# Optimization experiments

Measured on AMD Instinct MI355X. Metric: run time of the kernel, lower is better.

Reference implementation:

```python
import jax, jax.numpy as jnp
import numpy as np

K = 20          # neighbors
EPS = 1e-5      # BatchNorm eps
SLOPE = 0.2     # LeakyReLU negative slope


def setup_inputs() -> dict:
    key = jax.random.key(0)
    ks = jax.random.split(key, 6)
    B, C, N, O = 8, 3, 4096, 64
    x = jax.random.normal(ks[0], (B, C, N), dtype=jnp.float32)
    W = jax.random.normal(ks[1], (O, 2 * C), dtype=jnp.float32) * 0.1  # conv1x1 weight, bias=False
    gamma = 1.0 + 0.1 * jax.random.normal(ks[2], (O,), dtype=jnp.float32)
    beta = 0.1 * jax.random.normal(ks[3], (O,), dtype=jnp.float32)
    mean = 0.1 * jax.random.normal(ks[4], (O,), dtype=jnp.float32)
    var = jax.random.uniform(ks[5], (O,), dtype=jnp.float32, minval=0.5, maxval=1.5)
    return {"x": x, "W": W, "gamma": gamma, "beta": beta, "mean": mean, "var": var}


def reference(x, W, gamma, beta, mean, var):
    # x: [B, C, N]
    B, C, N = x.shape
    xt = jnp.swapaxes(x, 1, 2)                                   # [B, N, C]
    xx = jnp.sum(x * x, axis=1)                                  # [B, N]
    pd = 2.0 * jnp.einsum('bnc,bmc->bnm', xt, xt) - xx[:, :, None] - xx[:, None, :]
    _, idx = jax.lax.top_k(pd, K)                                # [B, N, K] nearest neighbors
    # gather neighbor features per batch
    feat = jax.vmap(lambda f, i: f[i])(xt, idx)                  # [B, N, K, C]
    center = xt[:, :, None, :]                                   # [B, N, 1, C]
    edge = jnp.concatenate(
        [feat - center, jnp.broadcast_to(center, feat.shape)], axis=-1)  # [B, N, K, 2C]
    # 1x1 conv == channel matmul
    y = jnp.einsum('bnkc,oc->bnko', edge, W)                     # [B, N, K, O]
    inv = gamma / jnp.sqrt(var + EPS)                            # fused inference BatchNorm
    y = y * inv + (beta - mean * inv)
    y = jnp.where(y >= 0, y, SLOPE * y)                          # LeakyReLU(0.2)
    y = jnp.max(y, axis=2)                                       # max over k -> [B, N, O]
    return jnp.swapaxes(y, 1, 2)                                 # [B, O, N]
```

## Files before the change

### kernel.cpp

```cpp
#include <hip/hip_runtime.h>
#include <math.h>

#define NPTS 4096
#define KNN  20
#define NOUT 64
#define WPB  8
#define QPW  2
#define QBLK (WPB * QPW)
#define BLKT (WPB * 64)
#define PCAP 96
#define HALF 2048

__device__ __forceinline__ unsigned ord32(float f) {
    unsigned u = __float_as_uint(f);
    int m = ((int)u) >> 31;
    return u ^ ((unsigned)m | 0x80000000u);
}
__device__ __forceinline__ float iord32(unsigned r) {
    unsigned u = (r & 0x80000000u) ? (r ^ 0x80000000u) : ~r;
    return __uint_as_float(u);
}
__device__ __forceinline__ int mbcnt64(unsigned long long m) {
    return __builtin_amdgcn_mbcnt_hi((unsigned)(m >> 32),
           __builtin_amdgcn_mbcnt_lo((unsigned)m, 0));
}

__global__ __launch_bounds__(256) void pack_kernel(const float* __restrict__ x,
                                                   float4* __restrict__ xq) {
    const int i = blockIdx.x * 256 + threadIdx.x;
    const int b = i >> 12, j = i & (NPTS - 1);
    const float* xb = x + (size_t)b * 3 * NPTS;
    const float a0 = xb[j], a1 = xb[NPTS + j], a2 = xb[2 * NPTS + j];
    xq[i] = make_float4(a0, a1, a2, -fmaf(a0, a0, fmaf(a1, a1, a2 * a2)));
}

__global__ __launch_bounds__(BLKT, 6) void edgeconv_kernel(
    const float4* __restrict__ xq,
    const float* __restrict__ Wm,
    const float* __restrict__ gamma,
    const float* __restrict__ beta,
    const float* __restrict__ mean,
    const float* __restrict__ var,
    float* __restrict__ out)
{
    const int bid = blockIdx.x;
    const int b   = bid >> 8;
    const int n0  = (bid & 255) * QBLK;
    const int t    = threadIdx.x;
    const int lane = t & 63;
    const int w    = t >> 6;

    __shared__ float4 tile[HALF];
    __shared__ unsigned long long pool[QBLK * PCAP];
    __shared__ int cnt[QBLK];

    const float4* xqb = xq + (size_t)b * NPTS;

    if (lane < QPW) cnt[QPW * w + lane] = 0;

    const int na = __builtin_amdgcn_readfirstlane(n0 + QPW * w);
    const float4 pva = xqb[na];
    const float4 pvb = xqb[na + 1];
    const float qa0 = 2.f * pva.x, qa1 = 2.f * pva.y, qa2 = 2.f * pva.z;
    const float qb0 = 2.f * pvb.x, qb1 = 2.f * pvb.y, qb2 = 2.f * pvb.z;

    float vma = -INFINITY, vmb = -INFINITY;

    #pragma unroll
    for (int k2 = 0; k2 < HALF / BLKT; ++k2) {
        const int c = t + k2 * BLKT;
        const float4 cc = xqb[c];
        tile[c] = cc;
        const float ea = fmaf(qa0, cc.x, fmaf(qa1, cc.y, fmaf(qa2, cc.z, cc.w)));
        const float eb = fmaf(qb0, cc.x, fmaf(qb1, cc.y, fmaf(qb2, cc.z, cc.w)));
        vma = fmaxf(vma, ea);
        vmb = fmaxf(vmb, eb);
    }

    #pragma unroll
    for (int g = 4; g < 8; ++g) {
        float4 cc[8];
        #pragma unroll
        for (int u = 0; u < 8; ++u) cc[u] = xqb[(g * 8 + u) * 64 + lane];
        #pragma unroll
        for (int u = 0; u < 8; ++u) {
            const float ea = fmaf(qa0, cc[u].x, fmaf(qa1, cc[u].y, fmaf(qa2, cc[u].z, cc[u].w)));
            const float eb = fmaf(qb0, cc[u].x, fmaf(qb1, cc[u].y, fmaf(qb2, cc[u].z, cc[u].w)));
            vma = fmaxf(vma, ea);
            vmb = fmaxf(vmb, eb);
        }
    }

    unsigned Ka = 0, Kb = 0;
    {
        const unsigned ka = ord32(vma), kb = ord32(vmb);
        #pragma unroll
        for (int bit = 31; bit >= 0; --bit) {
            const unsigned pa = Ka | (1u << bit);
            const unsigned pb = Kb | (1u << bit);
            const int ca = __popcll(__ballot(ka >= pa));
            const int cb = __popcll(__ballot(kb >= pb));
            if (ca >= KNN) Ka = pa;
            if (cb >= KNN) Kb = pb;
        }
    }
    const float Tfa = iord32(Ka);
    const float Tfb = iord32(Kb);

    __syncthreads();

    const int invl = (NPTS - 1) - lane;
    int* cnta = &cnt[QPW * w];
    int* cntb = &cnt[QPW * w + 1];
    unsigned long long* poola = pool + (size_t)(QPW * w) * PCAP;
    unsigned long long* poolb = pool + (size_t)(QPW * w + 1) * PCAP;

    #pragma unroll
    for (int g = 0; g < 4; ++g) {
        float4 cc[8];
        #pragma unroll
        for (int u = 0; u < 8; ++u) cc[u] = tile[(g * 8 + u) * 64 + lane];
        #pragma unroll
        for (int u = 0; u < 8; ++u) {
            const float ea = fmaf(qa0, cc[u].x, fmaf(qa1, cc[u].y, fmaf(qa2, cc[u].z, cc[u].w)));
            const float eb = fmaf(qb0, cc[u].x, fmaf(qb1, cc[u].y, fmaf(qb2, cc[u].z, cc[u].w)));
            const unsigned tag = (unsigned)(invl - (g * 8 + u) * 64);
            if (ea >= Tfa) {
                const int pos = atomicAdd(cnta, 1);
                if (pos < PCAP)
                    poola[pos] = ((unsigned long long)ord32(ea) << 32) | tag;
            }
            if (eb >= Tfb) {
                const int pos = atomicAdd(cntb, 1);
                if (pos < PCAP)
                    poolb[pos] = ((unsigned long long)ord32(eb) << 32) | tag;
            }
        }
    }

    #pragma unroll
    for (int g = 4; g < 8; ++g) {
        float4 cc[8];
        #pragma unroll
        for (int u = 0; u < 8; ++u) cc[u] = xqb[(g * 8 + u) * 64 + lane];
        #pragma unroll
        for (int u = 0; u < 8; ++u) {
            const float ea = fmaf(qa0, cc[u].x, fmaf(qa1, cc[u].y, fmaf(qa2, cc[u].z, cc[u].w)));
            const float eb = fmaf(qb0, cc[u].x, fmaf(qb1, cc[u].y, fmaf(qb2, cc[u].z, cc[u].w)));
            const unsigned tag = (unsigned)(invl - (g * 8 + u) * 64);
            if (ea >= Tfa) {
                const int pos = atomicAdd(cnta, 1);
                if (pos < PCAP)
                    poola[pos] = ((unsigned long long)ord32(ea) << 32) | tag;
            }
            if (eb >= Tfb) {
                const int pos = atomicAdd(cntb, 1);
                if (pos < PCAP)
                    poolb[pos] = ((unsigned long long)ord32(eb) << 32) | tag;
            }
        }
    }

    unsigned myidx[QPW];
    #pragma unroll
    for (int q = 0; q < QPW; ++q) {
        const int pr = QPW * w + q;
        unsigned long long* pl = pool + (size_t)pr * PCAP;
        int cw = __builtin_amdgcn_readfirstlane(cnt[pr]);
        if (cw > PCAP) cw = PCAP;

        const unsigned long long e0 = (lane < cw) ? pl[lane] : 0ull;
        const unsigned long long e1 = (lane + 64 < cw) ? pl[lane + 64] : 0ull;
        const unsigned k0 = (unsigned)(e0 >> 32), t0 = (unsigned)e0;
        const unsigned k1 = (unsigned)(e1 >> 32), t1 = (unsigned)e1;

        unsigned K = 0;
        #pragma unroll
        for (int bit = 31; bit >= 0; --bit) {
            const unsigned p = K | (1u << bit);
            const int c = __popcll(__ballot(k0 >= p)) + __popcll(__ballot(k1 >= p));
            if (c >= KNN) K = p;
        }

        unsigned long long g0 = __ballot(k0 > K);
        unsigned long long g1 = __ballot(k1 > K);
        const int m = __popcll(g0) + __popcll(g1);
        unsigned long long q0 = __ballot(k0 == K);
        unsigned long long q1 = __ballot(k1 == K);
        const int r = KNN - m;
        if (__popcll(q0) + __popcll(q1) > r) {
            unsigned TT = 0;
            #pragma unroll
            for (int bit = 11; bit >= 0; --bit) {
                const unsigned p = TT | (1u << bit);
                const int c = __popcll(__ballot(k0 == K && t0 >= p)) +
                              __popcll(__ballot(k1 == K && t1 >= p));
                if (c >= r) TT = p;
            }
            q0 = __ballot(k0 == K && t0 >= TT);
            q1 = __ballot(k1 == K && t1 >= TT);
        }

        unsigned* idxq = (unsigned*)pl;
        if ((g0 >> lane) & 1) idxq[mbcnt64(g0)] = t0;
        if ((g1 >> lane) & 1) idxq[__popcll(g0) + mbcnt64(g1)] = t1;
        if ((q0 >> lane) & 1) idxq[m + mbcnt64(q0)] = t0;
        if ((q1 >> lane) & 1) idxq[m + __popcll(q0) + mbcnt64(q1)] = t1;
        myidx[q] = idxq[(lane < KNN) ? lane : 0];
    }

    __syncthreads();

    const int o = lane;
    const float iv   = gamma[o] / sqrtf(var[o] + 1e-5f);
    const float bias = beta[o] - mean[o] * iv;
    const float* Wr = Wm + o * 6;
    const float w0p = Wr[0] * iv, w1p = Wr[1] * iv, w2p = Wr[2] * iv;
    const float w3p = Wr[3] * iv, w4p = Wr[4] * iv, w5p = Wr[5] * iv;
    const float basea = fmaf(w3p, pva.x, fmaf(w4p, pva.y, fmaf(w5p, pva.z, bias)));
    const float base2a = basea - fmaf(w0p, pva.x, fmaf(w1p, pva.y, w2p * pva.z));
    const float baseb = fmaf(w3p, pvb.x, fmaf(w4p, pvb.y, fmaf(w5p, pvb.z, bias)));
    const float base2b = baseb - fmaf(w0p, pvb.x, fmaf(w1p, pvb.y, w2p * pvb.z));

    float besta = -INFINITY, bestb = -INFINITY;
    #pragma unroll
    for (int k = 0; k < KNN; ++k) {
        const int lka = __builtin_amdgcn_readlane((int)myidx[0], k);
        const int lkb = __builtin_amdgcn_readlane((int)myidx[1], k);
        const int gia = __builtin_amdgcn_readfirstlane((NPTS - 1) - lka);
        const int gib = __builtin_amdgcn_readfirstlane((NPTS - 1) - lkb);
        const float4 fa = xqb[gia];
        const float4 fb = xqb[gib];
        float ya = fmaf(w0p, fa.x, fmaf(w1p, fa.y, fmaf(w2p, fa.z, base2a)));
        float yb = fmaf(w0p, fb.x, fmaf(w1p, fb.y, fmaf(w2p, fb.z, base2b)));
        ya = fmaxf(ya, 0.2f * ya);
        yb = fmaxf(yb, 0.2f * yb);
        besta = fmaxf(besta, ya);
        bestb = fmaxf(bestb, yb);
    }

    float* outT = (float*)pool;
    outT[o * (QBLK + 1) + QPW * w]     = besta;
    outT[o * (QBLK + 1) + QPW * w + 1] = bestb;
    __syncthreads();

    if (t < NOUT * 4) {
        const int oo = t >> 2, seg = t & 3;
        const int sb = oo * (QBLK + 1) + seg * 4;
        float4 vv;
        vv.x = outT[sb + 0]; vv.y = outT[sb + 1];
        vv.z = outT[sb + 2]; vv.w = outT[sb + 3];
        *(float4*)(out + ((size_t)b * NOUT + oo) * NPTS + n0 + seg * 4) = vv;
    }
}

extern "C" void kernel_launch(void* const* d_in, const int* in_sizes, int n_in,
                              void* d_out, int out_size, void* d_ws, size_t ws_size,
                              hipStream_t stream) {
    const float* x     = (const float*)d_in[0];
    const float* Wm    = (const float*)d_in[1];
    const float* gamma = (const float*)d_in[2];
    const float* beta  = (const float*)d_in[3];
    const float* mean  = (const float*)d_in[4];
    const float* var   = (const float*)d_in[5];
    float* out = (float*)d_out;
    float4* xq = (float4*)d_ws;

    const int B = in_sizes[0] / (3 * NPTS);
    pack_kernel<<<B * NPTS / 256, 256, 0, stream>>>(x, xq);
    const int nblocks = B * (NPTS / QBLK);
    edgeconv_kernel<<<nblocks, BLKT, 0, stream>>>(xq, Wm, gamma, beta, mean, var, out);
}
```

Before: 130.6 us.

## Process four queries per wave and tighten threshold estimation with finer buckets

Each wave now handles four query points instead of two, so every candidate load from LDS or global memory is reused across more distance evaluations, and the grid is halved. The threshold pre-pass keeps two partial maxima per lane (128 buckets) and runs the radix select on 16-bit truncated keys, which cuts the ballot iterations to 16. The LDS-staged half of the candidates shrinks to 1536 points. The extra per-query state raises register pressure. The coarser, truncated threshold may let more candidates into the fixed 96-entry pool, which risks overflow.

Result: slower. 136.6 us (+4.6%).

```diff
diff --git a/kernel.cpp b/kernel.cpp
--- a/kernel.cpp
+++ b/kernel.cpp
@@ -5,11 +5,11 @@
 #define KNN  20
 #define NOUT 64
 #define WPB  8
-#define QPW  2
+#define QPW  4
 #define QBLK (WPB * QPW)
 #define BLKT (WPB * 64)
 #define PCAP 96
-#define HALF 2048
+#define HALF 1536
 
 __device__ __forceinline__ unsigned ord32(float f) {
     unsigned u = __float_as_uint(f);
@@ -44,8 +44,8 @@
     float* __restrict__ out)
 {
     const int bid = blockIdx.x;
-    const int b   = bid >> 8;
-    const int n0  = (bid & 255) * QBLK;
+    const int b   = bid >> 7;
+    const int n0  = (bid & 127) * QBLK;
     const int t    = threadIdx.x;
     const int lane = t & 63;
     const int w    = t >> 6;
@@ -59,104 +59,102 @@
     if (lane < QPW) cnt[QPW * w + lane] = 0;
 
     const int na = __builtin_amdgcn_readfirstlane(n0 + QPW * w);
-    const float4 pva = xqb[na];
-    const float4 pvb = xqb[na + 1];
-    const float qa0 = 2.f * pva.x, qa1 = 2.f * pva.y, qa2 = 2.f * pva.z;
-    const float qb0 = 2.f * pvb.x, qb1 = 2.f * pvb.y, qb2 = 2.f * pvb.z;
-
-    float vma = -INFINITY, vmb = -INFINITY;
+    float q0[QPW], q1[QPW], q2[QPW];
+    #pragma unroll
+    for (int q = 0; q < QPW; ++q) {
+        const float4 pv = xqb[na + q];
+        q0[q] = 2.f * pv.x; q1[q] = 2.f * pv.y; q2[q] = 2.f * pv.z;
+    }
+
+    float vm0[QPW], vm1[QPW];
+    #pragma unroll
+    for (int q = 0; q < QPW; ++q) { vm0[q] = -INFINITY; vm1[q] = -INFINITY; }
 
     #pragma unroll
     for (int k2 = 0; k2 < HALF / BLKT; ++k2) {
         const int c = t + k2 * BLKT;
         const float4 cc = xqb[c];
         tile[c] = cc;
-        const float ea = fmaf(qa0, cc.x, fmaf(qa1, cc.y, fmaf(qa2, cc.z, cc.w)));
-        const float eb = fmaf(qb0, cc.x, fmaf(qb1, cc.y, fmaf(qb2, cc.z, cc.w)));
-        vma = fmaxf(vma, ea);
-        vmb = fmaxf(vmb, eb);
-    }
-
-    #pragma unroll
-    for (int g = 4; g < 8; ++g) {
-        float4 cc[8];
-        #pragma unroll
-        for (int u = 0; u < 8; ++u) cc[u] = xqb[(g * 8 + u) * 64 + lane];
-        #pragma unroll
-        for (int u = 0; u < 8; ++u) {
-            const float ea = fmaf(qa0, cc[u].x, fmaf(qa1, cc[u].y, fmaf(qa2, cc[u].z, cc[u].w)));
-            const float eb = fmaf(qb0, cc[u].x, fmaf(qb1, cc[u].y, fmaf(qb2, cc[u].z, cc[u].w)));
-            vma = fmaxf(vma, ea);
-            vmb = fmaxf(vmb, eb);
-        }
-    }
-
-    unsigned Ka = 0, Kb = 0;
-    {
-        const unsigned ka = ord32(vma), kb = ord32(vmb);
-        #pragma unroll
-        for (int bit = 31; bit >= 0; --bit) {
-            const unsigned pa = Ka | (1u << bit);
-            const unsigned pb = Kb | (1u << bit);
-            const int ca = __popcll(__ballot(ka >= pa));
-            const int cb = __popcll(__ballot(kb >= pb));
-            if (ca >= KNN) Ka = pa;
-            if (cb >= KNN) Kb = pb;
-        }
-    }
-    const float Tfa = iord32(Ka);
-    const float Tfb = iord32(Kb);
+        #pragma unroll
+        for (int q = 0; q < QPW; ++q) {
+            const float e = fmaf(q0[q], cc.x, fmaf(q1[q], cc.y, fmaf(q2[q], cc.z, cc.w)));
+            vm1[q] = fmaxf(vm1[q], e);
+        }
+    }
+
+    #pragma unroll
+    for (int g = 0; g < 10; ++g) {
+        float4 cc[4];
+        #pragma unroll
+        for (int u = 0; u < 4; ++u) cc[u] = xqb[HALF + (g * 4 + u) * 64 + lane];
+        #pragma unroll
+        for (int u = 0; u < 4; ++u) {
+            #pragma unroll
+            for (int q = 0; q < QPW; ++q) {
+                const float e = fmaf(q0[q], cc[u].x, fmaf(q1[q], cc[u].y, fmaf(q2[q], cc[u].z, cc[u].w)));
+                if (g < 5) vm0[q] = fmaxf(vm0[q], e);
+                else       vm1[q] = fmaxf(vm1[q], e);
+            }
+        }
+    }
+
+    float Tf[QPW];
+    #pragma unroll
+    for (int q = 0; q < QPW; ++q) {
+        const unsigned h0 = ord32(vm0[q]) >> 16;
+        const unsigned h1 = ord32(vm1[q]) >> 16;
+        unsigned K = 0;
+        #pragma unroll
+        for (int bit = 15; bit >= 0; --bit) {
+            const unsigned p = K | (1u << bit);
+            const int c = __popcll(__ballot(h0 >= p)) + __popcll(__ballot(h1 >= p));
+            if (c >= KNN) K = p;
+        }
+        Tf[q] = iord32(K << 16);
+    }
 
     __syncthreads();
 
     const int invl = (NPTS - 1) - lane;
-    int* cnta = &cnt[QPW * w];
-    int* cntb = &cnt[QPW * w + 1];
-    unsigned long long* poola = pool + (size_t)(QPW * w) * PCAP;
-    unsigned long long* poolb = pool + (size_t)(QPW * w + 1) * PCAP;
-
-    #pragma unroll
-    for (int g = 0; g < 4; ++g) {
-        float4 cc[8];
-        #pragma unroll
-        for (int u = 0; u < 8; ++u) cc[u] = tile[(g * 8 + u) * 64 + lane];
-        #pragma unroll
-        for (int u = 0; u < 8; ++u) {
-            const float ea = fmaf(qa0, cc[u].x, fmaf(qa1, cc[u].y, fmaf(qa2, cc[u].z, cc[u].w)));
-            const float eb = fmaf(qb0, cc[u].x, fmaf(qb1, cc[u].y, fmaf(qb2, cc[u].z, cc[u].w)));
-            const unsigned tag = (unsigned)(invl - (g * 8 + u) * 64);
-            if (ea >= Tfa) {
-                const int pos = atomicAdd(cnta, 1);
-                if (pos < PCAP)
-                    poola[pos] = ((unsigned long long)ord32(ea) << 32) | tag;
-            }
-            if (eb >= Tfb) {
-                const int pos = atomicAdd(cntb, 1);
-                if (pos < PCAP)
-                    poolb[pos] = ((unsigned long long)ord32(eb) << 32) | tag;
-            }
-        }
-    }
-
-    #pragma unroll
-    for (int g = 4; g < 8; ++g) {
-        float4 cc[8];
-        #pragma unroll
-        for (int u = 0; u < 8; ++u) cc[u] = xqb[(g * 8 + u) * 64 + lane];
-        #pragma unroll
-        for (int u = 0; u < 8; ++u) {
-            const float ea = fmaf(qa0, cc[u].x, fmaf(qa1, cc[u].y, fmaf(qa2, cc[u].z, cc[u].w)));
-            const float eb = fmaf(qb0, cc[u].x, fmaf(qb1, cc[u].y, fmaf(qb2, cc[u].z, cc[u].w)));
-            const unsigned tag = (unsigned)(invl - (g * 8 + u) * 64);
-            if (ea >= Tfa) {
-                const int pos = atomicAdd(cnta, 1);
-                if (pos < PCAP)
-                    poola[pos] = ((unsigned long long)ord32(ea) << 32) | tag;
-            }
-            if (eb >= Tfb) {
-                const int pos = atomicAdd(cntb, 1);
-                if (pos < PCAP)
-                    poolb[pos] = ((unsigned long long)ord32(eb) << 32) | tag;
+
+    #pragma unroll
+    for (int g = 0; g < 6; ++g) {
+        float4 cc[4];
+        #pragma unroll
+        for (int u = 0; u < 4; ++u) cc[u] = tile[(g * 4 + u) * 64 + lane];
+        #pragma unroll
+        for (int u = 0; u < 4; ++u) {
+            const unsigned tag = (unsigned)(invl - (g * 4 + u) * 64);
+            #pragma unroll
+            for (int q = 0; q < QPW; ++q) {
+                const float e = fmaf(q0[q], cc[u].x, fmaf(q1[q], cc[u].y, fmaf(q2[q], cc[u].z, cc[u].w)));
+                if (e >= Tf[q]) {
+                    const int pos = atomicAdd(&cnt[QPW * w + q], 1);
+                    if (pos < PCAP)
+                        pool[(QPW * w + q) * PCAP + pos] =
+                            ((unsigned long long)ord32(e) << 32) | tag;
+                }
+            }
+        }
+    }
+
+    #pragma unroll
+    for (int g = 0; g < 10; ++g) {
+        float4 cc[4];
+        #pragma unroll
+        for (int u = 0; u < 4; ++u) cc[u] = xqb[HALF + (g * 4 + u) * 64 + lane];
+        #pragma unroll
+        for (int u = 0; u < 4; ++u) {
+            const unsigned tag = (unsigned)(invl - HALF - (g * 4 + u) * 64);
+            #pragma unroll
+            for (int q = 0; q < QPW; ++q) {
+                const float e = fmaf(q0[q], cc[u].x, fmaf(q1[q], cc[u].y, fmaf(q2[q], cc[u].z, cc[u].w)));
+                if (e >= Tf[q]) {
+                    const int pos = atomicAdd(&cnt[QPW * w + q], 1);
+                    if (pos < PCAP)
+                        pool[(QPW * w + q) * PCAP + pos] =
+                            ((unsigned long long)ord32(e) << 32) | tag;
+                }
             }
         }
     }
@@ -185,10 +183,10 @@
         unsigned long long g0 = __ballot(k0 > K);
         unsigned long long g1 = __ballot(k1 > K);
         const int m = __popcll(g0) + __popcll(g1);
-        unsigned long long q0 = __ballot(k0 == K);
-        unsigned long long q1 = __ballot(k1 == K);
+        unsigned long long s0 = __ballot(k0 == K);
+        unsigned long long s1 = __ballot(k1 == K);
         const int r = KNN - m;
-        if (__popcll(q0) + __popcll(q1) > r) {
+        if (__popcll(s0) + __popcll(s1) > r) {
             unsigned TT = 0;
             #pragma unroll
             for (int bit = 11; bit >= 0; --bit) {
@@ -197,15 +195,15 @@
                               __popcll(__ballot(k1 == K && t1 >= p));
                 if (c >= r) TT = p;
             }
-            q0 = __ballot(k0 == K && t0 >= TT);
-            q1 = __ballot(k1 == K && t1 >= TT);
+            s0 = __ballot(k0 == K && t0 >= TT);
+            s1 = __ballot(k1 == K && t1 >= TT);
         }
 
         unsigned* idxq = (unsigned*)pl;
         if ((g0 >> lane) & 1) idxq[mbcnt64(g0)] = t0;
         if ((g1 >> lane) & 1) idxq[__popcll(g0) + mbcnt64(g1)] = t1;
-        if ((q0 >> lane) & 1) idxq[m + mbcnt64(q0)] = t0;
-        if ((q1 >> lane) & 1) idxq[m + __popcll(q0) + mbcnt64(q1)] = t1;
+        if ((s0 >> lane) & 1) idxq[m + mbcnt64(s0)] = t0;
+        if ((s1 >> lane) & 1) idxq[m + __popcll(s0) + mbcnt64(s1)] = t1;
         myidx[q] = idxq[(lane < KNN) ? lane : 0];
     }
 
@@ -217,35 +215,29 @@
     const float* Wr = Wm + o * 6;
     const float w0p = Wr[0] * iv, w1p = Wr[1] * iv, w2p = Wr[2] * iv;
     const float w3p = Wr[3] * iv, w4p = Wr[4] * iv, w5p = Wr[5] * iv;
-    const float basea = fmaf(w3p, pva.x, fmaf(w4p, pva.y, fmaf(w5p, pva.z, bias)));
-    const float base2a = basea - fmaf(w0p, pva.x, fmaf(w1p, pva.y, w2p * pva.z));
-    const float baseb = fmaf(w3p, pvb.x, fmaf(w4p, pvb.y, fmaf(w5p, pvb.z, bias)));
-    const float base2b = baseb - fmaf(w0p, pvb.x, fmaf(w1p, pvb.y, w2p * pvb.z));
-
-    float besta = -INFINITY, bestb = -INFINITY;
-    #pragma unroll
-    for (int k = 0; k < KNN; ++k) {
-        const int lka = __builtin_amdgcn_readlane((int)myidx[0], k);
-        const int lkb = __builtin_amdgcn_readlane((int)myidx[1], k);
-        const int gia = __builtin_amdgcn_readfirstlane((NPTS - 1) - lka);
-        const int gib = __builtin_amdgcn_readfirstlane((NPTS - 1) - lkb);
-        const float4 fa = xqb[gia];
-        const float4 fb = xqb[gib];
-        float ya = fmaf(w0p, fa.x, fmaf(w1p, fa.y, fmaf(w2p, fa.z, base2a)));
-        float yb = fmaf(w0p, fb.x, fmaf(w1p, fb.y, fmaf(w2p, fb.z, base2b)));
-        ya = fmaxf(ya, 0.2f * ya);
-        yb = fmaxf(yb, 0.2f * yb);
-        besta = fmaxf(besta, ya);
-        bestb = fmaxf(bestb, yb);
-    }
 
     float* outT = (float*)pool;
-    outT[o * (QBLK + 1) + QPW * w]     = besta;
-    outT[o * (QBLK + 1) + QPW * w + 1] = bestb;
+    #pragma unroll
+    for (int q = 0; q < QPW; ++q) {
+        const float4 pv = xqb[na + q];
+        const float basep = fmaf(w3p, pv.x, fmaf(w4p, pv.y, fmaf(w5p, pv.z, bias)));
+        const float base2 = basep - fmaf(w0p, pv.x, fmaf(w1p, pv.y, w2p * pv.z));
+        float best = -INFINITY;
+        #pragma unroll
+        for (int k = 0; k < KNN; ++k) {
+            const int lk = __builtin_amdgcn_readlane((int)myidx[q], k);
+            const int gi = __builtin_amdgcn_readfirstlane((NPTS - 1) - lk);
+            const float4 f = xqb[gi];
+            float y = fmaf(w0p, f.x, fmaf(w1p, f.y, fmaf(w2p, f.z, base2)));
+            y = fmaxf(y, 0.2f * y);
+            best = fmaxf(best, y);
+        }
+        outT[o * (QBLK + 1) + QPW * w + q] = best;
+    }
     __syncthreads();
 
-    if (t < NOUT * 4) {
-        const int oo = t >> 2, seg = t & 3;
+    {
+        const int oo = t >> 3, seg = t & 7;
         const int sb = oo * (QBLK + 1) + seg * 4;
         float4 vv;
         vv.x = outT[sb + 0]; vv.y = outT[sb + 1];
```
